# Kernel optimization log

Measured on AMD Instinct MI355X. Metric: run time of the kernel, lower is better.

## Reference

```python
import jax, jax.numpy as jnp
import numpy as np

N = 30          # time steps
K = 100.0       # strike
ALPHA = 0.5     # expectile level
B = 1048576     # batch size


def setup_inputs() -> dict:
    key = jax.random.key(0)
    k1, k2, k3, k4, k5 = jax.random.split(key, 5)
    delta_pred = jax.random.normal(k1, (B, 2 * (N - 2)), dtype=jnp.float32)
    batch_x = jax.random.normal(k2, (B, 2), dtype=jnp.float32)
    # Heston price paths ~ around the strike K=100 so the call clamp is active for ~half the paths
    S1 = jax.random.uniform(k3, (B, N + 1), dtype=jnp.float32) * 20.0 + 90.0
    S2 = jax.random.uniform(k4, (B, N + 1), dtype=jnp.float32) * 20.0 + 90.0
    w = jax.random.normal(k5, (), dtype=jnp.float32)  # model.w scalar risk level
    return {"delta_pred": delta_pred, "batch_x": batch_x, "S1": S1, "S2": S2, "w": w}


def reference(delta_pred, batch_x, S1, S2, w):
    # Original interleaves S1/S2 into S1_S2 (even cols = S1, odd cols = S2).
    # First hedging step uses batch_x; remaining n-2 steps use delta_pred.
    sum_delta_S = batch_x[:, 0] * (S1[:, 1] - S1[:, 0]) + batch_x[:, 1] * (S2[:, 1] - S2[:, 0])
    d1 = delta_pred[:, 0::2]               # [B, n-2], hedges on asset 1
    d2 = delta_pred[:, 1::2]               # [B, n-2], hedges on asset 2
    dS1 = S1[:, 2:N] - S1[:, 1:N - 1]      # [B, n-2] price increments
    dS2 = S2[:, 2:N] - S2[:, 1:N - 1]
    sum_delta_S = sum_delta_S + jnp.sum(d1 * dS1 + d2 * dS2, axis=1)
    liabilities = jnp.maximum(S1[:, -1] - K, 0.0)  # call payoff on S1 terminal price
    loss = w + jnp.maximum(liabilities - sum_delta_S - w, 0.0) / (1.0 - ALPHA)
    return jnp.mean(loss)
```

## Files before the change

### kernel.cpp

```cpp
#include <hip/hip_runtime.h>

#define NROWS    1048576
#define TILE     32
#define NBLOCKS  2048
#define NTHREADS 256
#define TILES_PER_BLOCK 16

#define DP_TILE_B (TILE * 224)
#define S_TILE_B  (TILE * 124)
#define BX_TILE_B (TILE * 8)

#define LDS_DP 0
#define LDS_S1 7168
#define LDS_S2 11136
#define LDS_BX 15104
#define BUF_B  15360

#define GLDS16(g, l) __builtin_amdgcn_global_load_lds(                         \
    (const __attribute__((address_space(1))) void*)(g),                        \
    (__attribute__((address_space(3))) void*)(l), 16, 0, 0)
#define GLDS4(g, l) __builtin_amdgcn_global_load_lds(                          \
    (const __attribute__((address_space(1))) void*)(g),                        \
    (__attribute__((address_space(3))) void*)(l), 4, 0, 0)

__device__ __forceinline__ void stage_tile(unsigned char* buf,
    const char* dpg, const char* s1g, const char* s2g, const char* bxg,
    int wv, int lane)
{
    if (wv == 0) {
        #pragma unroll
        for (int c = 0; c < 4; ++c)
            GLDS16(dpg + c * 1024 + lane * 16, buf + LDS_DP + c * 1024);
    } else if (wv == 1) {
        #pragma unroll
        for (int c = 4; c < 7; ++c)
            GLDS16(dpg + c * 1024 + lane * 16, buf + LDS_DP + c * 1024);
        GLDS4(bxg + lane * 4, buf + LDS_BX);
    } else if (wv == 2) {
        #pragma unroll
        for (int c = 0; c < 3; ++c)
            GLDS16(s1g + c * 1024 + lane * 16, buf + LDS_S1 + c * 1024);
        GLDS4(s1g + 3072 + lane * 4, buf + LDS_S1 + 3072);
        GLDS4(s1g + 3328 + lane * 4, buf + LDS_S1 + 3328);
        GLDS4(s1g + 3584 + lane * 4, buf + LDS_S1 + 3584);
        GLDS4(s1g + 3712 + lane * 4, buf + LDS_S1 + 3712);
    } else {
        #pragma unroll
        for (int c = 0; c < 3; ++c)
            GLDS16(s2g + c * 1024 + lane * 16, buf + LDS_S2 + c * 1024);
        GLDS4(s2g + 3072 + lane * 4, buf + LDS_S2 + 3072);
        GLDS4(s2g + 3328 + lane * 4, buf + LDS_S2 + 3328);
        GLDS4(s2g + 3584 + lane * 4, buf + LDS_S2 + 3584);
        GLDS4(s2g + 3712 + lane * 4, buf + LDS_S2 + 3712);
    }
}

__device__ __forceinline__ void wait_own_prefetch(int wv)
{
    if (wv < 2) asm volatile("s_waitcnt vmcnt(4)" ::: "memory");
    else        asm volatile("s_waitcnt vmcnt(7)" ::: "memory");
}

__device__ __forceinline__ void compute_tile(const unsigned char* buf,
    int row, int seg, float w, double& acc)
{
    const float*  s1row = (const float*)(buf + LDS_S1 + row * 124);
    const float*  s2row = (const float*)(buf + LDS_S2 + row * 124);
    const float2* dprow = (const float2*)(buf + LDS_DP + row * 224);
    const float2  b2    = *(const float2*)(buf + LDS_BX + row * 8);

    const int sb = 7 * seg;
    float s1v[9], s2v[9];
    #pragma unroll
    for (int i = 0; i < 9; ++i) { s1v[i] = s1row[sb + i]; s2v[i] = s2row[sb + i]; }

    float sum = 0.0f;
    #pragma unroll
    for (int u = 0; u < 7; ++u) {
        const float2 d = dprow[sb + u];
        sum += d.x * (s1v[u + 2] - s1v[u + 1]) + d.y * (s2v[u + 2] - s2v[u + 1]);
    }
    const float t0 = b2.x * (s1v[1] - s1v[0]) + b2.y * (s2v[1] - s2v[0]);
    sum += (seg == 0) ? t0 : 0.0f;

    sum += __shfl_xor(sum, 1);
    sum += __shfl_xor(sum, 2);

    const float liab = fmaxf(s1row[30] - 100.0f, 0.0f);
    const float loss = w + fmaxf(liab - sum - w, 0.0f) * 2.0f;
    if (seg == 0) acc += (double)loss;
}

__global__ __launch_bounds__(NTHREADS) void loss_pipe_kernel(
    const float* __restrict__ dp, const float* __restrict__ bx,
    const float* __restrict__ S1, const float* __restrict__ S2,
    const float* __restrict__ wp, double* __restrict__ partial)
{
    __shared__ __align__(16) unsigned char lds[2 * BUF_B];
    __shared__ double sm[NTHREADS];

    const int tid  = threadIdx.x;
    const int lane = tid & 63;
    const int wv   = tid >> 6;
    const int row  = (tid & 127) >> 2;
    const int seg  = tid & 3;
    const float w  = *wp;

    const long tile0 = (long)blockIdx.x * TILES_PER_BLOCK;
    double acc = 0.0;

    stage_tile(lds,
               (const char*)dp + tile0 * DP_TILE_B,
               (const char*)S1 + tile0 * S_TILE_B,
               (const char*)S2 + tile0 * S_TILE_B,
               (const char*)bx + tile0 * BX_TILE_B, wv, lane);

    for (int t = 0; t < TILES_PER_BLOCK - 1; ++t) {
        const long nt = tile0 + t + 1;
        stage_tile(lds + ((t + 1) & 1) * BUF_B,
                   (const char*)dp + nt * DP_TILE_B,
                   (const char*)S1 + nt * S_TILE_B,
                   (const char*)S2 + nt * S_TILE_B,
                   (const char*)bx + nt * BX_TILE_B, wv, lane);
        wait_own_prefetch(wv);
        __builtin_amdgcn_s_barrier();
        if (tid < 128) compute_tile(lds + (t & 1) * BUF_B, row, seg, w, acc);
        __builtin_amdgcn_s_barrier();
    }
    asm volatile("s_waitcnt vmcnt(0)" ::: "memory");
    __builtin_amdgcn_s_barrier();
    if (tid < 128)
        compute_tile(lds + ((TILES_PER_BLOCK - 1) & 1) * BUF_B, row, seg, w, acc);

    sm[tid] = acc;
    __syncthreads();
    #pragma unroll
    for (int s = NTHREADS / 2; s > 0; s >>= 1) {
        if (tid < s) sm[tid] += sm[tid + s];
        __syncthreads();
    }
    if (tid == 0) partial[blockIdx.x] = sm[0];
}

__global__ __launch_bounds__(NTHREADS) void loss_final_kernel(
    const double* __restrict__ partial, float* __restrict__ out)
{
    double acc = 0.0;
    for (int i = threadIdx.x; i < NBLOCKS; i += NTHREADS) acc += partial[i];
    __shared__ double sm[NTHREADS];
    sm[threadIdx.x] = acc;
    __syncthreads();
    #pragma unroll
    for (int s = NTHREADS / 2; s > 0; s >>= 1) {
        if (threadIdx.x < s) sm[threadIdx.x] += sm[threadIdx.x + s];
        __syncthreads();
    }
    if (threadIdx.x == 0) out[0] = (float)(sm[0] / (double)NROWS);
}

extern "C" void kernel_launch(void* const* d_in, const int* in_sizes, int n_in,
                              void* d_out, int out_size, void* d_ws, size_t ws_size,
                              hipStream_t stream)
{
    const float* dp = (const float*)d_in[0];
    const float* bx = (const float*)d_in[1];
    const float* S1 = (const float*)d_in[2];
    const float* S2 = (const float*)d_in[3];
    const float* w  = (const float*)d_in[4];

    double* partial = (double*)d_ws;
    float* out = (float*)d_out;

    loss_pipe_kernel<<<NBLOCKS, NTHREADS, 0, stream>>>(dp, bx, S1, S2, w, partial);
    loss_final_kernel<<<1, NTHREADS, 0, stream>>>(partial, out);
}
```

Measured before the change: 95.32 us.

## Triple-buffer LDS tile pipeline and fuse final reduction via last-block atomic counter

Measured after the change: 275.0 us. 2.88x slower.

```diff
diff --git a/kernel.cpp b/kernel.cpp
--- a/kernel.cpp
+++ b/kernel.cpp
@@ -55,12 +55,6 @@
     }
 }
 
-__device__ __forceinline__ void wait_own_prefetch(int wv)
-{
-    if (wv < 2) asm volatile("s_waitcnt vmcnt(4)" ::: "memory");
-    else        asm volatile("s_waitcnt vmcnt(7)" ::: "memory");
-}
-
 __device__ __forceinline__ void compute_tile(const unsigned char* buf,
     int row, int seg, float w, double& acc)
 {
@@ -94,10 +88,12 @@
 __global__ __launch_bounds__(NTHREADS) void loss_pipe_kernel(
     const float* __restrict__ dp, const float* __restrict__ bx,
     const float* __restrict__ S1, const float* __restrict__ S2,
-    const float* __restrict__ wp, double* __restrict__ partial)
+    const float* __restrict__ wp, double* __restrict__ partial,
+    unsigned int* __restrict__ counter, float* __restrict__ out)
 {
-    __shared__ __align__(16) unsigned char lds[2 * BUF_B];
+    __shared__ __align__(16) unsigned char lds[3 * BUF_B];
     __shared__ double sm[NTHREADS];
+    __shared__ int last_flag;
 
     const int tid  = threadIdx.x;
     const int lane = tid & 63;
@@ -109,28 +105,35 @@
     const long tile0 = (long)blockIdx.x * TILES_PER_BLOCK;
     double acc = 0.0;
 
-    stage_tile(lds,
-               (const char*)dp + tile0 * DP_TILE_B,
-               (const char*)S1 + tile0 * S_TILE_B,
-               (const char*)S2 + tile0 * S_TILE_B,
-               (const char*)bx + tile0 * BX_TILE_B, wv, lane);
+    #pragma unroll
+    for (int p = 0; p < 2; ++p)
+        stage_tile(lds + p * BUF_B,
+                   (const char*)dp + (tile0 + p) * DP_TILE_B,
+                   (const char*)S1 + (tile0 + p) * S_TILE_B,
+                   (const char*)S2 + (tile0 + p) * S_TILE_B,
+                   (const char*)bx + (tile0 + p) * BX_TILE_B, wv, lane);
 
-    for (int t = 0; t < TILES_PER_BLOCK - 1; ++t) {
-        const long nt = tile0 + t + 1;
-        stage_tile(lds + ((t + 1) & 1) * BUF_B,
-                   (const char*)dp + nt * DP_TILE_B,
-                   (const char*)S1 + nt * S_TILE_B,
-                   (const char*)S2 + nt * S_TILE_B,
-                   (const char*)bx + nt * BX_TILE_B, wv, lane);
-        wait_own_prefetch(wv);
+    int cb = 0;
+    for (int t = 0; t < TILES_PER_BLOCK; ++t) {
+        if (t < TILES_PER_BLOCK - 1) {
+            if (wv < 2) asm volatile("s_waitcnt vmcnt(4)" ::: "memory");
+            else        asm volatile("s_waitcnt vmcnt(7)" ::: "memory");
+        } else {
+            asm volatile("s_waitcnt vmcnt(0)" ::: "memory");
+        }
         __builtin_amdgcn_s_barrier();
-        if (tid < 128) compute_tile(lds + (t & 1) * BUF_B, row, seg, w, acc);
-        __builtin_amdgcn_s_barrier();
+        if (t + 2 < TILES_PER_BLOCK) {
+            const long nt = tile0 + t + 2;
+            const int nb = (cb + 2 >= 3) ? cb - 1 : cb + 2;
+            stage_tile(lds + nb * BUF_B,
+                       (const char*)dp + nt * DP_TILE_B,
+                       (const char*)S1 + nt * S_TILE_B,
+                       (const char*)S2 + nt * S_TILE_B,
+                       (const char*)bx + nt * BX_TILE_B, wv, lane);
+        }
+        if (tid < 128) compute_tile(lds + cb * BUF_B, row, seg, w, acc);
+        cb = (cb == 2) ? 0 : cb + 1;
     }
-    asm volatile("s_waitcnt vmcnt(0)" ::: "memory");
-    __builtin_amdgcn_s_barrier();
-    if (tid < 128)
-        compute_tile(lds + ((TILES_PER_BLOCK - 1) & 1) * BUF_B, row, seg, w, acc);
 
     sm[tid] = acc;
     __syncthreads();
@@ -139,23 +142,31 @@
         if (tid < s) sm[tid] += sm[tid + s];
         __syncthreads();
     }
-    if (tid == 0) partial[blockIdx.x] = sm[0];
-}
 
-__global__ __launch_bounds__(NTHREADS) void loss_final_kernel(
-    const double* __restrict__ partial, float* __restrict__ out)
-{
-    double acc = 0.0;
-    for (int i = threadIdx.x; i < NBLOCKS; i += NTHREADS) acc += partial[i];
-    __shared__ double sm[NTHREADS];
-    sm[threadIdx.x] = acc;
+    if (tid == 0) {
+        __hip_atomic_store(&partial[blockIdx.x], sm[0],
+                           __ATOMIC_RELEASE, __HIP_MEMORY_SCOPE_AGENT);
+        const unsigned int old = __hip_atomic_fetch_add(counter, 1u,
+                           __ATOMIC_ACQ_REL, __HIP_MEMORY_SCOPE_AGENT);
+        last_flag = (old == NBLOCKS - 1) ? 1 : 0;
+    }
     __syncthreads();
-    #pragma unroll
-    for (int s = NTHREADS / 2; s > 0; s >>= 1) {
-        if (threadIdx.x < s) sm[threadIdx.x] += sm[threadIdx.x + s];
+    if (last_flag) {
+        double a = 0.0;
+        #pragma unroll
+        for (int k = 0; k < NBLOCKS / NTHREADS; ++k)
+            a += __hip_atomic_load(&partial[tid * (NBLOCKS / NTHREADS) + k],
+                                   __ATOMIC_RELAXED, __HIP_MEMORY_SCOPE_AGENT);
         __syncthreads();
+        sm[tid] = a;
+        __syncthreads();
+        #pragma unroll
+        for (int s = NTHREADS / 2; s > 0; s >>= 1) {
+            if (tid < s) sm[tid] += sm[tid + s];
+            __syncthreads();
+        }
+        if (tid == 0) out[0] = (float)(sm[0] / (double)NROWS);
     }
-    if (threadIdx.x == 0) out[0] = (float)(sm[0] / (double)NROWS);
 }
 
 extern "C" void kernel_launch(void* const* d_in, const int* in_sizes, int n_in,
@@ -169,8 +180,11 @@
     const float* w  = (const float*)d_in[4];
 
     double* partial = (double*)d_ws;
+    unsigned int* counter =
+        (unsigned int*)((char*)d_ws + NBLOCKS * sizeof(double));
     float* out = (float*)d_out;
 
-    loss_pipe_kernel<<<NBLOCKS, NTHREADS, 0, stream>>>(dp, bx, S1, S2, w, partial);
-    loss_final_kernel<<<1, NTHREADS, 0, stream>>>(partial, out);
+    hipMemsetAsync(counter, 0, sizeof(unsigned int), stream);
+    loss_pipe_kernel<<<NBLOCKS, NTHREADS, 0, stream>>>(
+        dp, bx, S1, S2, w, partial, counter, out);
 }
```
